# Kernel optimization log

Measured on AMD Instinct MI355X. Metric: run time of the kernel, lower is better.

The kernel has to match this reference:

```python
import jax, jax.numpy as jnp
import numpy as np

N = 50000      # nodes
E = 800000     # edges (before self-loops)
F_IN = 256     # feature_size
H = 96         # hidden_channels
G = 64         # graphs in batch
NC = 4         # num_classes
EPS = 1e-5     # BatchNorm eps


def _lrelu(x, s=0.01):
    return jnp.where(x >= 0, x, s * x)


def _gat(x, W, a_s, a_d, b, src, dst):
    # PyG GATConv, heads=1: linear transform, edge-wise LeakyReLU(0.2) scores,
    # segment softmax over destination nodes, scatter-add aggregation.
    h = x @ W                                                  # [N,H]
    e = _lrelu((h * a_s).sum(-1)[src] + (h * a_d).sum(-1)[dst], 0.2)  # [E+N]
    m = jax.ops.segment_max(e, dst, num_segments=N)
    ee = jnp.exp(e - m[dst])
    denom = jax.ops.segment_sum(ee, dst, num_segments=N)
    alpha = ee / denom[dst]
    return jax.ops.segment_sum(alpha[:, None] * h[src], dst, num_segments=N) + b


def _bn(x, g, b):
    # training-mode BatchNorm over the node dimension
    mu = x.mean(0)
    var = ((x - mu) ** 2).mean(0)
    return g * (x - mu) / jnp.sqrt(var + EPS) + b


def setup_inputs() -> dict:
    key = jax.random.key(0)
    ks = jax.random.split(key, 20)
    p = lambda i, sh: jax.random.normal(ks[i], sh, jnp.float32) * 0.05
    inp = {
        "x": jax.random.normal(ks[0], (N, F_IN), jnp.float32),
        "edge_index": jax.random.randint(ks[1], (2, E), 0, N),
        "batch": jnp.sort(jax.random.randint(ks[2], (N,), 0, G)),
        "embed_W": p(3, (F_IN, H)), "embed_b": jnp.zeros((H,), jnp.float32),
        "conv1_W": p(4, (H, H)), "conv1_as": p(5, (H,)), "conv1_ad": p(6, (H,)), "conv1_b": jnp.zeros((H,), jnp.float32),
        "conv2_W": p(7, (H, H)), "conv2_as": p(8, (H,)), "conv2_ad": p(9, (H,)), "conv2_b": jnp.zeros((H,), jnp.float32),
        "conv3_W": p(10, (H, H)), "conv3_as": p(11, (H,)), "conv3_ad": p(12, (H,)), "conv3_b": jnp.zeros((H,), jnp.float32),
        "fc1_W": p(13, (H, H)), "fc1_b": jnp.zeros((H,), jnp.float32),
        "fc2_W": p(14, (H, H)), "fc2_b": jnp.zeros((H,), jnp.float32),
        "bn1_g": jnp.ones((H,), jnp.float32), "bn1_b": jnp.zeros((H,), jnp.float32),
        "bn2_g": jnp.ones((H,), jnp.float32), "bn2_b": jnp.zeros((H,), jnp.float32),
        "bn3_g": jnp.ones((H,), jnp.float32), "bn3_b": jnp.zeros((H,), jnp.float32),
        "fc3_W": p(15, (H, H // 2)), "fc3_b": jnp.zeros((H // 2,), jnp.float32),
        "fc4_W": p(16, (H // 2, NC)), "fc4_b": jnp.zeros((NC,), jnp.float32),
    }
    return inp


def reference(x, edge_index, batch, embed_W, embed_b,
              conv1_W, conv1_as, conv1_ad, conv1_b,
              conv2_W, conv2_as, conv2_ad, conv2_b,
              conv3_W, conv3_as, conv3_ad, conv3_b,
              fc1_W, fc1_b, fc2_W, fc2_b,
              bn1_g, bn1_b, bn2_g, bn2_b, bn3_g, bn3_b,
              fc3_W, fc3_b, fc4_W, fc4_b):
    loops = jnp.arange(N)
    src = jnp.concatenate([edge_index[0], loops])   # GATConv add_self_loops=True
    dst = jnp.concatenate([edge_index[1], loops])

    h = _lrelu(x @ embed_W + embed_b)
    identity = h
    h = _lrelu(_bn(_gat(h, conv1_W, conv1_as, conv1_ad, conv1_b, src, dst), bn1_g, bn1_b)) + identity
    h = _lrelu(h @ fc1_W + fc1_b)
    h = _lrelu(_bn(_gat(h, conv2_W, conv2_as, conv2_ad, conv2_b, src, dst), bn2_g, bn2_b)) + identity
    h = _lrelu(h @ fc2_W + fc2_b)
    h = _lrelu(_bn(_gat(h, conv3_W, conv3_as, conv3_ad, conv3_b, src, dst), bn3_g, bn3_b)) + identity

    # Poincare ball expmap0 with c=1: tanh(||u||) * u / ||u||
    n = jnp.maximum(jnp.linalg.norm(h, axis=-1, keepdims=True), 1e-15)
    h = jnp.tanh(n) * h / n

    cnt = jax.ops.segment_sum(jnp.ones((N,), h.dtype), batch, num_segments=G)
    pooled = jax.ops.segment_sum(h, batch, num_segments=G) / jnp.maximum(cnt, 1.0)[:, None]

    o = _lrelu(pooled @ fc3_W + fc3_b)
    return o @ fc4_W + fc4_b
```

## Files before the change

### kernel.cpp

```cpp
#include <hip/hip_runtime.h>
#include <hip/hip_bf16.h>

#define DEVINL __device__ __forceinline__

constexpr int N_NODES = 50000;
constexpr int N_EDGES = 800000;
constexpr int F_IN    = 256;
constexpr int H       = 96;
constexpr int NG      = 64;
constexpr float BN_EPS = 1e-5f;
constexpr int SLOT    = 64;
constexpr int NREP    = 8;
constexpr int REPSZ   = NG * H + NG;
constexpr int BNREP   = 64;

constexpr int NBLK1 = 160;
constexpr int EPT1  = N_EDGES / NBLK1;
constexpr int NBUCK = 391;
constexpr int BCAP  = 64;
constexpr int NPACK = 276;

typedef short bf16x8 __attribute__((ext_vector_type(8)));
typedef float f32x4  __attribute__((ext_vector_type(4)));
typedef unsigned int u32x4 __attribute__((ext_vector_type(4)));

DEVINL float bf2f(unsigned int u) {
    union { unsigned int i; float f; } c; c.i = u << 16; return c.f;
}
DEVINL unsigned short f2bf(float f) {
    union { float f; unsigned int i; } c; c.f = f;
    unsigned int x = c.i;
    return (unsigned short)((x + 0x7fffu + ((x >> 16) & 1u)) >> 16);
}
DEVINL float lrelu01(float v) { return v >= 0.f ? v : 0.01f * v; }
DEVINL float ldf(const void* p, size_t i, int f32) {
    return f32 ? ((const float*)p)[i] : bf2f(((const unsigned short*)p)[i]);
}
DEVINL u32x4 ntld4(const void* p) {
    return __builtin_nontemporal_load((const u32x4*)p);
}

__global__ __launch_bounds__(256) void setup_k(
    const unsigned short* __restrict__ x,
    int* __restrict__ flag,
    const int* __restrict__ ei, uint2* __restrict__ bbuf,
    int* __restrict__ bcnt,
    const void* __restrict__ sE, const void* __restrict__ s0,
    const void* __restrict__ s1, const void* __restrict__ s2,
    const void* __restrict__ s3, const void* __restrict__ s4,
    unsigned short* __restrict__ dE, unsigned short* __restrict__ d0,
    unsigned short* __restrict__ d1, unsigned short* __restrict__ d2,
    unsigned short* __restrict__ d3, unsigned short* __restrict__ d4)
{
    __shared__ int lcur[NBUCK];

    if ((int)blockIdx.x >= NPACK) {
        int blk = (int)blockIdx.x - NPACK;
        for (int i = threadIdx.x; i < NBUCK; i += 256) lcur[i] = 0;
        __syncthreads();
        int base = blk * EPT1;
        int end  = base + EPT1;
        for (int e = base + (int)threadIdx.x; e < end; e += 256) {
            int sv = __builtin_nontemporal_load(ei + e);
            int dv = __builtin_nontemporal_load(ei + N_EDGES + e);
            int b  = dv >> 7;
            int pos = atomicAdd(&lcur[b], 1);
            if (pos < BCAP)
                bbuf[((size_t)blk * NBUCK + b) * BCAP + pos] =
                    make_uint2((unsigned)sv, (unsigned)dv);
        }
        __syncthreads();
        for (int i = threadIdx.x; i < NBUCK; i += 256)
            bcnt[blk * NBUCK + i] = min(lcur[i], BCAP);
        return;
    }

    if (blockIdx.x == 0 && threadIdx.x < 64) {
        int l = threadIdx.x;
        float f = bf2f(x[l]);
        bool huge = !(fabsf(f) <= 1e4f);
        unsigned long long m = __ballot(huge);
        if (l == 0) flag[0] = (__popcll(m) >= 8) ? 1 : 0;
    }
    float ff = bf2f(x[threadIdx.x & 63]);
    bool huge = !(fabsf(ff) <= 1e4f);
    unsigned long long mm = __ballot(huge);
    int lf32 = (__popcll(mm) >= 8) ? 1 : 0;

    int bb = blockIdx.x;
    const void* src; unsigned short* dst; int K, i0;
    if (bb < 96) { src = sE; dst = dE; K = F_IN; i0 = bb * 256; }
    else {
        int m = (bb - 96) / 36, r = (bb - 96) % 36;
        K = H; i0 = r * 256;
        if      (m == 0) { src = s0; dst = d0; }
        else if (m == 1) { src = s1; dst = d1; }
        else if (m == 2) { src = s2; dst = d2; }
        else if (m == 3) { src = s3; dst = d3; }
        else             { src = s4; dst = d4; }
    }
    int i = i0 + threadIdx.x;
    if (i >= K * 96) return;
    int c   = i / 3072;
    int rem = i - c * 3072;
    int t    = rem >> 9;
    int rem2 = rem & 511;
    int l = rem2 >> 3, j = rem2 & 7;
    int k = c * 32 + (l >> 4) * 8 + j;
    int n = t * 16 + (l & 15);
    if (lf32) dst[i] = f2bf(((const float*)src)[k * 96 + n]);
    else      dst[i] = ((const unsigned short*)src)[k * 96 + n];
}

__global__ __launch_bounds__(256, 4) void embconv_k(
    const void* __restrict__ xp, const unsigned short* __restrict__ WpkE,
    const void* __restrict__ embB, const unsigned short* __restrict__ Wcv,
    const int* __restrict__ dflag,
    unsigned short* __restrict__ ident, unsigned short* __restrict__ out,
    const void* __restrict__ as_, const void* __restrict__ ad_,
    float* __restrict__ s, float* __restrict__ d,
    const uint2* __restrict__ bbuf, const int* __restrict__ bcnt,
    unsigned short* __restrict__ col, int* __restrict__ fill,
    float* __restrict__ bnsumR, int M)
{
    union SMem {
        struct {
            unsigned short slots[128][SLOT];
            int lcnt[128];
            int ccnt[NBLK1];
        } c;
        unsigned short R[64][104];
    };
    __shared__ SMem sm;

    {
        int zi = blockIdx.x * 256 + threadIdx.x;
        if (zi < BNREP * 192) bnsumR[zi] = 0.f;
    }

    if ((int)blockIdx.x < NBUCK) {
        int b = blockIdx.x, tid = threadIdx.x;
        if (tid < 128) sm.c.lcnt[tid] = 0;
        for (int i = tid; i < NBLK1; i += 256) sm.c.ccnt[i] = bcnt[i * NBUCK + b];
        __syncthreads();

        int n0 = b << 7;
        for (int g = tid; g < NBLK1 * BCAP; g += 256) {
            int blk = g >> 6;
            int i   = g & (BCAP - 1);
            if (i < sm.c.ccnt[blk]) {
                uint2 e = bbuf[((size_t)blk * NBUCK + b) * BCAP + i];
                int local = (int)e.y - n0;
                int slot = atomicAdd(&sm.c.lcnt[local], 1);
                if (slot < SLOT) sm.c.slots[local][slot] = (unsigned short)e.x;
            }
        }
        __syncthreads();

        const uint4* ls = (const uint4*)sm.c.slots;
        for (int i = tid; i < 128 * 8; i += 256) {
            int node = n0 + (i >> 3);
            if (node < N_NODES)
                ((uint4*)col)[(size_t)node * 8 + (i & 7)] = ls[i];
        }
        if (tid < 128) {
            int node = n0 + tid;
            if (node < N_NODES) fill[node] = sm.c.lcnt[tid];
        }
        return;
    }

    const int gb   = (int)blockIdx.x - NBUCK;
    const int f32  = dflag[0];
    const int l    = threadIdx.x & 63;
    const int wave = threadIdx.x >> 6;
    const int row0 = gb * 64 + wave * 16;
    const int m    = l & 15;
    const int q    = l >> 4;
    const int arow = row0 + m;
    const bool aok = arow < M;

    bf16x8 av[8];
    #pragma unroll
    for (int c = 0; c < 8; c++) {
        bf16x8 a = {};
        if (aok) {
            if (f32) {
                const float* A = (const float*)xp + (size_t)arow * F_IN + c * 32 + q * 8;
                u32x4 u0 = ntld4(A);
                u32x4 u1 = ntld4(A + 4);
                #pragma unroll
                for (int j = 0; j < 4; j++) a[j]     = (short)f2bf(__uint_as_float(u0[j]));
                #pragma unroll
                for (int j = 0; j < 4; j++) a[4 + j] = (short)f2bf(__uint_as_float(u1[j]));
            } else {
                union { u32x4 u; bf16x8 h; } cv;
                cv.u = ntld4((const unsigned short*)xp + (size_t)arow * F_IN + c * 32 + q * 8);
                a = cv.h;
            }
        }
        av[c] = a;
    }

    f32x4 acc[6] = {};
    const bf16x8* wp1 = (const bf16x8*)WpkE;
    #pragma unroll
    for (int c = 0; c < 8; c++) {
        const int base = c * 384 + l;
        #pragma unroll
        for (int t = 0; t < 6; t++)
            acc[t] = __builtin_amdgcn_mfma_f32_16x16x32_bf16(av[c], wp1[base + t * 64], acc[t], 0, 0, 0);
    }

    float bv[6];
    #pragma unroll
    for (int t = 0; t < 6; t++) bv[t] = ldf(embB, t * 16 + m, f32);
    #pragma unroll
    for (int r = 0; r < 4; r++) {
        int lr = wave * 16 + q * 4 + r;
        int rr = row0 + q * 4 + r;
        #pragma unroll
        for (int t = 0; t < 6; t++) {
            unsigned short sv = f2bf(lrelu01(acc[t][r] + bv[t]));
            sm.R[lr][t * 16 + m] = sv;
            if (rr < M) ident[(size_t)rr * 96 + m + t * 16] = sv;
        }
    }
    __syncthreads();

    bf16x8 a2[3];
    #pragma unroll
    for (int c = 0; c < 3; c++)
        a2[c] = *(const bf16x8*)&sm.R[wave * 16 + m][c * 32 + q * 8];

    f32x4 acc2[6] = {};
    const bf16x8* wp2 = (const bf16x8*)Wcv;
    #pragma unroll
    for (int c = 0; c < 3; c++) {
        const int base = c * 384 + l;
        #pragma unroll
        for (int t = 0; t < 6; t++)
            acc2[t] = __builtin_amdgcn_mfma_f32_16x16x32_bf16(a2[c], wp2[base + t * 64], acc2[t], 0, 0, 0);
    }

    #pragma unroll
    for (int r = 0; r < 4; r++) {
        int rr = row0 + q * 4 + r;
        if (rr >= M) continue;
        size_t o = (size_t)rr * 96 + m;
        #pragma unroll
        for (int t = 0; t < 6; t++)
            out[o + t * 16] = f2bf(acc2[t][r]);
    }

    float asv[6], adv[6];
    #pragma unroll
    for (int t = 0; t < 6; t++) {
        asv[t] = ldf(as_, t * 16 + m, f32);
        adv[t] = ldf(ad_, t * 16 + m, f32);
    }
    #pragma unroll
    for (int r = 0; r < 4; r++) {
        float ps = 0.f, pd = 0.f;
        #pragma unroll
        for (int t = 0; t < 6; t++) {
            ps = fmaf(acc2[t][r], asv[t], ps);
            pd = fmaf(acc2[t][r], adv[t], pd);
        }
        #pragma unroll
        for (int off = 1; off < 16; off <<= 1) {
            ps += __shfl_xor(ps, off);
            pd += __shfl_xor(pd, off);
        }
        int rr = row0 + q * 4 + r;
        if (m == 0 && rr < M) { s[rr] = ps; d[rr] = pd; }
    }
}

__global__ __launch_bounds__(256, 4) void fcconv_k(
    const unsigned short* __restrict__ Ap,
    const unsigned short* __restrict__ Wfc, const void* __restrict__ bfc,
    const unsigned short* __restrict__ Wcv,
    const int* __restrict__ dflag,
    unsigned short* __restrict__ out,
    const void* __restrict__ as_, const void* __restrict__ ad_,
    float* __restrict__ s, float* __restrict__ d,
    const float* __restrict__ coefp, const unsigned short* __restrict__ idn,
    float* __restrict__ bnsumR, int M)
{
    __shared__ unsigned short R[64][104];

    {
        int zi = blockIdx.x * 256 + threadIdx.x;
        if (zi < BNREP * 192) bnsumR[zi] = 0.f;
    }

    const int wf32 = dflag[0];
    const int l    = threadIdx.x & 63;
    const int wave = threadIdx.x >> 6;
    const int row0 = blockIdx.x * 64 + wave * 16;
    const int m    = l & 15;
    const int q    = l >> 4;
    const int arow = row0 + m;
    const bool aok = arow < M;

    bf16x8 av[3];
    #pragma unroll
    for (int c = 0; c < 3; c++) {
        bf16x8 a = {};
        if (aok) {
            const int f0 = c * 32 + q * 8;
            uint4 xu = *(const uint4*)(Ap  + (size_t)arow * H + f0);
            uint4 iu = *(const uint4*)(idn + (size_t)arow * H + f0);
            unsigned int xs[4] = { xu.x, xu.y, xu.z, xu.w };
            unsigned int is[4] = { iu.x, iu.y, iu.z, iu.w };
            #pragma unroll
            for (int jj = 0; jj < 4; jj++) {
                int f = f0 + 2 * jj;
                float v0 = lrelu01(bf2f(xs[jj] & 0xffff) * coefp[f]     + coefp[96 + f])     + bf2f(is[jj] & 0xffff);
                float v1 = lrelu01(bf2f(xs[jj] >> 16)    * coefp[f + 1] + coefp[96 + f + 1]) + bf2f(is[jj] >> 16);
                a[2 * jj]     = (short)f2bf(v0);
                a[2 * jj + 1] = (short)f2bf(v1);
            }
        }
        av[c] = a;
    }

    f32x4 acc[6] = {};
    const bf16x8* wp1 = (const bf16x8*)Wfc;
    #pragma unroll
    for (int c = 0; c < 3; c++) {
        const int base = c * 384 + l;
        #pragma unroll
        for (int t = 0; t < 6; t++)
            acc[t] = __builtin_amdgcn_mfma_f32_16x16x32_bf16(av[c], wp1[base + t * 64], acc[t], 0, 0, 0);
    }

    float bv[6];
    #pragma unroll
    for (int t = 0; t < 6; t++) bv[t] = ldf(bfc, t * 16 + m, wf32);
    #pragma unroll
    for (int r = 0; r < 4; r++) {
        int lr = wave * 16 + q * 4 + r;
        #pragma unroll
        for (int t = 0; t < 6; t++)
            R[lr][t * 16 + m] = f2bf(lrelu01(acc[t][r] + bv[t]));
    }
    __syncthreads();

    bf16x8 a2[3];
    #pragma unroll
    for (int c = 0; c < 3; c++)
        a2[c] = *(const bf16x8*)&R[wave * 16 + m][c * 32 + q * 8];

    f32x4 acc2[6] = {};
    const bf16x8* wp2 = (const bf16x8*)Wcv;
    #pragma unroll
    for (int c = 0; c < 3; c++) {
        const int base = c * 384 + l;
        #pragma unroll
        for (int t = 0; t < 6; t++)
            acc2[t] = __builtin_amdgcn_mfma_f32_16x16x32_bf16(a2[c], wp2[base + t * 64], acc2[t], 0, 0, 0);
    }

    #pragma unroll
    for (int r = 0; r < 4; r++) {
        int rr = row0 + q * 4 + r;
        if (rr >= M) continue;
        size_t o = (size_t)rr * 96 + m;
        #pragma unroll
        for (int t = 0; t < 6; t++)
            out[o + t * 16] = f2bf(acc2[t][r]);
    }

    float asv[6], adv[6];
    #pragma unroll
    for (int t = 0; t < 6; t++) {
        asv[t] = ldf(as_, t * 16 + m, wf32);
        adv[t] = ldf(ad_, t * 16 + m, wf32);
    }
    #pragma unroll
    for (int r = 0; r < 4; r++) {
        float ps = 0.f, pd = 0.f;
        #pragma unroll
        for (int t = 0; t < 6; t++) {
            ps = fmaf(acc2[t][r], asv[t], ps);
            pd = fmaf(acc2[t][r], adv[t], pd);
        }
        #pragma unroll
        for (int off = 1; off < 16; off <<= 1) {
            ps += __shfl_xor(ps, off);
            pd += __shfl_xor(pd, off);
        }
        int rr = row0 + q * 4 + r;
        if (m == 0 && rr < M) { s[rr] = ps; d[rr] = pd; }
    }
}

__global__ __launch_bounds__(256) void agg_k(
    const unsigned short* __restrict__ h2, const float* __restrict__ s,
    const float* __restrict__ d, const int* __restrict__ fill,
    const unsigned short* __restrict__ col, const void* __restrict__ bias,
    const int* __restrict__ dflag, unsigned short* __restrict__ out,
    float* __restrict__ bnsumR, float* __restrict__ zp, int M)
{
    __shared__ uint2 uwb[4][80];
    __shared__ float lstat[4][192];
    if (zp) {
        int zi = blockIdx.x * 256 + threadIdx.x;
        if (zi < NREP * REPSZ) zp[zi] = 0.f;
    }
    int f32 = dflag[0];
    int v = (blockIdx.x * blockDim.x + threadIdx.x) >> 6;
    int l = threadIdx.x & 63;
    int wv = threadIdx.x >> 6;
    bool act = v < M;
    bool hw = (l < 48);
    int  c2 = 2 * l;
    float o0 = 0.f, o1 = 0.f;

    if (act) {
        int st   = v * SLOT;
        int degr = min(fill[v], SLOT - 1);
        int deg  = degr + 1;

        float dv = d[v];
        int u = 0; float e = -1e30f;
        if (l < degr) {
            u = col[st + l];
            float t = s[u] + dv;
            e = t >= 0.f ? t : 0.2f * t;
        } else if (l == degr) {
            u = v;
            float t = s[v] + dv;
            e = t >= 0.f ? t : 0.2f * t;
        }
        float lm = e;
        #pragma unroll
        for (int off = 32; off > 0; off >>= 1) lm = fmaxf(lm, __shfl_xor(lm, off));
        float w = (l < deg) ? __expf(e - lm) : 0.f;
        float lsum = w;
        #pragma unroll
        for (int off = 32; off > 0; off >>= 1) lsum += __shfl_xor(lsum, off);
        float rden = 1.0f / lsum;

        uwb[wv][l] = make_uint2((unsigned int)u, __float_as_uint(w));
        if (l < 16) uwb[wv][64 + l] = make_uint2(0u, 0u);

        float a0 = 0.f, a1 = 0.f;
        const uint2* myuw = uwb[wv];
        for (int j = 0; j < deg; j += 16) {
            int lim = deg - j;
            uint2 p[16];
            #pragma unroll
            for (int k = 0; k < 16; k++) p[k] = myuw[j + k];
            if (hw) {
                unsigned int hv[16];
                #pragma unroll
                for (int k = 0; k < 16; k++)
                    hv[k] = (k < lim) ? *(const unsigned int*)(h2 + (size_t)p[k].x * 96 + c2) : 0u;
                #pragma unroll
                for (int k = 0; k < 16; k++) {
                    float wj = __uint_as_float(p[k].y);
                    a0 = fmaf(wj, bf2f(hv[k] & 0xffff), a0);
                    a1 = fmaf(wj, bf2f(hv[k] >> 16),    a1);
                }
            }
        }
        if (hw) {
            float b0 = ldf(bias, c2,     f32);
            float b1 = ldf(bias, c2 + 1, f32);
            unsigned int o = (unsigned int)f2bf(a0 * rden + b0)
                           | ((unsigned int)f2bf(a1 * rden + b1) << 16);
            *(unsigned int*)(out + (size_t)v * 96 + c2) = o;
            o0 = bf2f(o & 0xffff);
            o1 = bf2f(o >> 16);
        }
    }

    if (hw) {
        lstat[wv][c2]          = o0;
        lstat[wv][c2 + 1]      = o1;
        lstat[wv][96 + c2]     = o0 * o0;
        lstat[wv][97 + c2]     = o1 * o1;
    }
    __syncthreads();
    if (threadIdx.x < 192) {
        float tot = lstat[0][threadIdx.x] + lstat[1][threadIdx.x]
                  + lstat[2][threadIdx.x] + lstat[3][threadIdx.x];
        atomicAdd(&bnsumR[(blockIdx.x & (BNREP - 1)) * 192 + threadIdx.x], tot);
    }
}

__global__ void bncoef_k(const float* __restrict__ bnsumR,
                         const void* __restrict__ g_,
                         const void* __restrict__ b_,
                         const int* __restrict__ dflag,
                         float* __restrict__ coef)
{
    __shared__ float tot[192];
    int t = threadIdx.x;
    if (t < 192) {
        float s = 0.f;
        #pragma unroll 8
        for (int r = 0; r < BNREP; r++) s += bnsumR[r * 192 + t];
        tot[t] = s;
    }
    __syncthreads();
    if (t < 96) {
        int f32 = dflag[0];
        float mu  = tot[t] * (1.f / N_NODES);
        float var = tot[96 + t] * (1.f / N_NODES) - mu * mu;
        float rinv = 1.0f / sqrtf(var + BN_EPS);
        float sc = ldf(g_, t, f32) * rinv;
        coef[t]      = sc;
        coef[96 + t] = ldf(b_, t, f32) - mu * sc;
    }
}

__global__ __launch_bounds__(256) void bnpool_k(
    const unsigned short* __restrict__ h, const float* __restrict__ coef,
    const unsigned short* __restrict__ iden, const int* __restrict__ batch,
    float* __restrict__ pooled8, int M)
{
    int w = (blockIdx.x * blockDim.x + threadIdx.x) >> 6;
    int l = threadIdx.x & 63;
    int v0 = w * 16;
    if (v0 >= M) return;
    float* P = pooled8 + (blockIdx.x & (NREP - 1)) * REPSZ;
    float* C = P + NG * H;
    bool hw = (l < 48);
    int  c2 = 2 * l;
    float sc0 = 0.f, sc1 = 0.f, sh0 = 0.f, sh1 = 0.f;
    if (hw) {
        sc0 = coef[c2]; sc1 = coef[c2 + 1];
        sh0 = coef[96 + c2]; sh1 = coef[97 + c2];
    }
    int nv = min(16, M - v0);

    int gb[16];
    #pragma unroll
    for (int k = 0; k < 16; k++) gb[k] = batch[v0 + min(k, nv - 1)];

    float x0[16], x1[16], q[16];
    #pragma unroll
    for (int k = 0; k < 16; k++) { x0[k] = 0.f; x1[k] = 0.f; q[k] = 0.f; }
    if (hw) {
        unsigned int xu[16], iu[16];
        #pragma unroll
        for (int k = 0; k < 16; k++) {
            int v = v0 + k;
            if (k < nv) {
                xu[k] = *(const unsigned int*)(h    + (size_t)v * 96 + c2);
                iu[k] = *(const unsigned int*)(iden + (size_t)v * 96 + c2);
            } else { xu[k] = 0u; iu[k] = 0u; }
        }
        #pragma unroll
        for (int k = 0; k < 16; k++) {
            x0[k] = lrelu01(bf2f(xu[k] & 0xffff) * sc0 + sh0) + bf2f(iu[k] & 0xffff);
            x1[k] = lrelu01(bf2f(xu[k] >> 16)    * sc1 + sh1) + bf2f(iu[k] >> 16);
            q[k]  = x0[k] * x0[k] + x1[k] * x1[k];
        }
    }

    #pragma unroll
    for (int off = 32; off > 0; off >>= 1) {
        #pragma unroll
        for (int k = 0; k < 16; k++) q[k] += __shfl_xor(q[k], off);
    }

    float f[16];
    #pragma unroll
    for (int k = 0; k < 16; k++) {
        float n = fmaxf(sqrtf(q[k]), 1e-15f);
        if (n < 15.f) {
            float t = __expf(2.f * n);
            f[k] = (t - 1.f) / ((t + 1.f) * n);
        } else {
            f[k] = 1.f / n;
        }
    }

    float a0 = 0.f, a1 = 0.f, cnt = 0.f;
    int curg = -1;
    for (int k = 0; k < nv; k++) {
        int g = gb[k];
        if (g != curg) {
            if (curg >= 0) {
                if (hw) {
                    atomicAdd(&P[curg * 96 + c2],     a0);
                    atomicAdd(&P[curg * 96 + c2 + 1], a1);
                }
                if (l == 0) atomicAdd(&C[curg], cnt);
            }
            a0 = a1 = 0.f; cnt = 0.f; curg = g;
        }
        a0 = fmaf(f[k], x0[k], a0);
        a1 = fmaf(f[k], x1[k], a1);
        cnt += 1.f;
    }
    if (curg >= 0) {
        if (hw) {
            atomicAdd(&P[curg * 96 + c2],     a0);
            atomicAdd(&P[curg * 96 + c2 + 1], a1);
        }
        if (l == 0) atomicAdd(&C[curg], cnt);
    }
}

__global__ __launch_bounds__(64) void head_k(const float* __restrict__ pooled8,
                                             const void* __restrict__ w3,
                                             const void* __restrict__ b3,
                                             const void* __restrict__ w4,
                                             const void* __restrict__ b4,
                                             const int* __restrict__ dflag,
                                             void* __restrict__ outv)
{
    int g = blockIdx.x;
    int t = threadIdx.x;
    int f32 = dflag[0];
    __shared__ float p[96];
    __shared__ float o[48];
    float cs = 0.f;
    #pragma unroll
    for (int r = 0; r < NREP; r++) cs += pooled8[r * REPSZ + NG * H + g];
    float inv = 1.0f / fmaxf(cs, 1.0f);
    for (int c = t; c < 96; c += 64) {
        float v = 0.f;
        #pragma unroll
        for (int r = 0; r < NREP; r++) v += pooled8[r * REPSZ + g * 96 + c];
        p[c] = v * inv;
    }
    __syncthreads();
    if (t < 48) {
        float a = ldf(b3, t, f32);
        #pragma unroll
        for (int c = 0; c < 96; c++) a = fmaf(p[c], ldf(w3, (size_t)c * 48 + t, f32), a);
        o[t] = lrelu01(a);
    }
    __syncthreads();
    if (t < 4) {
        float a = ldf(b4, t, f32);
        #pragma unroll
        for (int j = 0; j < 48; j++) a = fmaf(o[j], ldf(w4, j * 4 + t, f32), a);
        if (f32) ((float*)outv)[g * 4 + t] = a;
        else     ((unsigned short*)outv)[g * 4 + t] = f2bf(a);
    }
}

extern "C" void kernel_launch(void* const* d_in, const int* in_sizes, int n_in,
                              void* d_out, int out_size, void* d_ws, size_t ws_size,
                              hipStream_t stream)
{
    const void* x     = d_in[0];
    const int*  ei    = (const int*)d_in[1];
    const int*  batch = (const int*)d_in[2];
    const void* embW  = d_in[3];
    const void* embB  = d_in[4];
    const void* convW[3]  = { d_in[5],  d_in[9],  d_in[13] };
    const void* convAs[3] = { d_in[6],  d_in[10], d_in[14] };
    const void* convAd[3] = { d_in[7],  d_in[11], d_in[15] };
    const void* convB[3]  = { d_in[8],  d_in[12], d_in[16] };
    const void* fcW[2]    = { d_in[17], d_in[19] };
    const void* fcB[2]    = { d_in[18], d_in[20] };
    const void* bnG[3]    = { d_in[21], d_in[23], d_in[25] };
    const void* bnB[3]    = { d_in[22], d_in[24], d_in[26] };
    const void* fc3W = d_in[27];
    const void* fc3b = d_in[28];
    const void* fc4W = d_in[29];
    const void* fc4b = d_in[30];

    char* wp_ = (char*)d_ws;
    auto alloc = [&](size_t b) { char* p = wp_; wp_ += (b + 255) & ~(size_t)255; return p; };
    int*   dflag = (int*)alloc(256);
    unsigned short* ident = (unsigned short*)alloc((size_t)N_NODES * H * 2);
    unsigned short* hA    = (unsigned short*)alloc((size_t)N_NODES * H * 2);
    unsigned short* hB    = (unsigned short*)alloc((size_t)N_NODES * H * 2);
    float* s_sc  = (float*)alloc((size_t)N_NODES * 4);
    float* d_sc  = (float*)alloc((size_t)N_NODES * 4);
    float* bnsumR = (float*)alloc((size_t)BNREP * 192 * 4);
    float* coef  = (float*)alloc(192 * 4);
    float* pooled8 = (float*)alloc((size_t)NREP * REPSZ * 4);
    int*   fill  = (int*)alloc((size_t)N_NODES * 4);
    unsigned short* col = (unsigned short*)alloc((size_t)N_NODES * SLOT * 2);
    uint2* bbuf = (uint2*)alloc((size_t)NBLK1 * NBUCK * BCAP * 8);
    int*   bcnt = (int*)alloc((size_t)NBLK1 * NBUCK * 4);
    unsigned short* wpkEmb = (unsigned short*)alloc((size_t)F_IN * 96 * 2);
    unsigned short* wpkS[5];
    for (int i = 0; i < 5; i++) wpkS[i] = (unsigned short*)alloc((size_t)H * 96 * 2);

    const int GM = (N_NODES + 63) / 64;
    const int GW = (N_NODES * 64 + 255) / 256;
    const int GP = ((N_NODES + 15) / 16 * 64 + 255) / 256;

    setup_k<<<NPACK + NBLK1, 256, 0, stream>>>(
        (const unsigned short*)x, dflag,
        ei, bbuf, bcnt,
        embW, convW[0], convW[1], convW[2], fcW[0], fcW[1],
        wpkEmb, wpkS[0], wpkS[1], wpkS[2], wpkS[3], wpkS[4]);

    embconv_k<<<NBUCK + GM, 256, 0, stream>>>(
        x, wpkEmb, embB, wpkS[0], dflag, ident, hB,
        convAs[0], convAd[0], s_sc, d_sc,
        bbuf, bcnt, col, fill, bnsumR, N_NODES);

    agg_k<<<GW, 256, 0, stream>>>(hB, s_sc, d_sc, fill, col, convB[0], dflag, hA,
                                  bnsumR, nullptr, N_NODES);
    bncoef_k<<<1, 192, 0, stream>>>(bnsumR, bnG[0], bnB[0], dflag, coef);
    fcconv_k<<<GM, 256, 0, stream>>>(hA, wpkS[3], fcB[0], wpkS[1], dflag, hB,
                                     convAs[1], convAd[1], s_sc, d_sc,
                                     coef, ident, bnsumR, N_NODES);

    agg_k<<<GW, 256, 0, stream>>>(hB, s_sc, d_sc, fill, col, convB[1], dflag, hA,
                                  bnsumR, nullptr, N_NODES);
    bncoef_k<<<1, 192, 0, stream>>>(bnsumR, bnG[1], bnB[1], dflag, coef);
    fcconv_k<<<GM, 256, 0, stream>>>(hA, wpkS[4], fcB[1], wpkS[2], dflag, hB,
                                     convAs[2], convAd[2], s_sc, d_sc,
                                     coef, ident, bnsumR, N_NODES);

    agg_k<<<GW, 256, 0, stream>>>(hB, s_sc, d_sc, fill, col, convB[2], dflag, hA,
                                  bnsumR, pooled8, N_NODES);
    bncoef_k<<<1, 192, 0, stream>>>(bnsumR, bnG[2], bnB[2], dflag, coef);

    bnpool_k<<<GP, 256, 0, stream>>>(hA, coef, ident, batch, pooled8, N_NODES);
    head_k<<<NG, 64, 0, stream>>>(pooled8, fc3W, fc3b, fc4W, fc4b, dflag, d_out);
}
```

Measured before the change: 356.7 us.

## Fold BN coefficient kernel into consumers and broadcast edge weights via shuffles

Removes the three single-block bncoef_k launches: each fcconv_k and bnpool_k block now reduces the replicated BN partial sums and computes scale/shift into shared memory. The BN sum buffers are double-buffered so a consumer can read the previous layer's sums while zeroing the next layer's buffer. In agg_k, neighbor indices and softmax weights are broadcast with wave shuffles instead of being staged through shared memory, and the self-loop handling is merged into one branch. The trade-off is redundant per-block reduction of 64x192 floats plus extra barriers in every consumer block, in exchange for fewer launches and serial gaps.

```diff
diff --git a/kernel.cpp b/kernel.cpp
--- a/kernel.cpp
+++ b/kernel.cpp
@@ -38,6 +38,31 @@
 }
 DEVINL u32x4 ntld4(const void* p) {
     return __builtin_nontemporal_load((const u32x4*)p);
+}
+
+DEVINL void coef_from_sums(float* lcoef, const float* __restrict__ bnsumRd,
+                           const void* __restrict__ g_, const void* __restrict__ b_,
+                           int f32)
+{
+    int t = threadIdx.x;
+    if (t < 192) {
+        float ssum = 0.f;
+        #pragma unroll 8
+        for (int r = 0; r < BNREP; r++) ssum += bnsumRd[r * 192 + t];
+        lcoef[t] = ssum;
+    }
+    __syncthreads();
+    float sc = 0.f, sh = 0.f;
+    if (t < 96) {
+        float mu  = lcoef[t] * (1.f / N_NODES);
+        float var = lcoef[96 + t] * (1.f / N_NODES) - mu * mu;
+        float rinv = 1.0f / sqrtf(var + BN_EPS);
+        sc = ldf(g_, t, f32) * rinv;
+        sh = ldf(b_, t, f32) - mu * sc;
+    }
+    __syncthreads();
+    if (t < 96) { lcoef[t] = sc; lcoef[96 + t] = sh; }
+    __syncthreads();
 }
 
 __global__ __launch_bounds__(256) void setup_k(
@@ -121,7 +146,7 @@
     float* __restrict__ s, float* __restrict__ d,
     const uint2* __restrict__ bbuf, const int* __restrict__ bcnt,
     unsigned short* __restrict__ col, int* __restrict__ fill,
-    float* __restrict__ bnsumR, int M)
+    float* __restrict__ bnsumZ, int M)
 {
     union SMem {
         struct {
@@ -135,7 +160,7 @@
 
     {
         int zi = blockIdx.x * 256 + threadIdx.x;
-        if (zi < BNREP * 192) bnsumR[zi] = 0.f;
+        if (zi < BNREP * 192) bnsumZ[zi] = 0.f;
     }
 
     if ((int)blockIdx.x < NBUCK) {
@@ -285,17 +310,22 @@
     unsigned short* __restrict__ out,
     const void* __restrict__ as_, const void* __restrict__ ad_,
     float* __restrict__ s, float* __restrict__ d,
-    const float* __restrict__ coefp, const unsigned short* __restrict__ idn,
-    float* __restrict__ bnsumR, int M)
+    const void* __restrict__ g_, const void* __restrict__ b_,
+    const float* __restrict__ bnsumRd,
+    const unsigned short* __restrict__ idn,
+    float* __restrict__ bnsumZ, int M)
 {
     __shared__ unsigned short R[64][104];
+    __shared__ float lcoef[192];
 
     {
         int zi = blockIdx.x * 256 + threadIdx.x;
-        if (zi < BNREP * 192) bnsumR[zi] = 0.f;
+        if (zi < BNREP * 192) bnsumZ[zi] = 0.f;
     }
 
     const int wf32 = dflag[0];
+    coef_from_sums(lcoef, bnsumRd, g_, b_, wf32);
+
     const int l    = threadIdx.x & 63;
     const int wave = threadIdx.x >> 6;
     const int row0 = blockIdx.x * 64 + wave * 16;
@@ -317,8 +347,8 @@
             #pragma unroll
             for (int jj = 0; jj < 4; jj++) {
                 int f = f0 + 2 * jj;
-                float v0 = lrelu01(bf2f(xs[jj] & 0xffff) * coefp[f]     + coefp[96 + f])     + bf2f(is[jj] & 0xffff);
-                float v1 = lrelu01(bf2f(xs[jj] >> 16)    * coefp[f + 1] + coefp[96 + f + 1]) + bf2f(is[jj] >> 16);
+                float v0 = lrelu01(bf2f(xs[jj] & 0xffff) * lcoef[f]     + lcoef[96 + f])     + bf2f(is[jj] & 0xffff);
+                float v1 = lrelu01(bf2f(xs[jj] >> 16)    * lcoef[f + 1] + lcoef[97 + f]) + bf2f(is[jj] >> 16);
                 a[2 * jj]     = (short)f2bf(v0);
                 a[2 * jj + 1] = (short)f2bf(v1);
             }
@@ -404,7 +434,6 @@
     const int* __restrict__ dflag, unsigned short* __restrict__ out,
     float* __restrict__ bnsumR, float* __restrict__ zp, int M)
 {
-    __shared__ uint2 uwb[4][80];
     __shared__ float lstat[4][192];
     if (zp) {
         int zi = blockIdx.x * 256 + threadIdx.x;
@@ -425,14 +454,11 @@
         int deg  = degr + 1;
 
         float dv = d[v];
-        int u = 0; float e = -1e30f;
-        if (l < degr) {
-            u = col[st + l];
+        int u = v;
+        if (l < degr) u = col[st + l];
+        float e = -1e30f;
+        if (l < deg) {
             float t = s[u] + dv;
-            e = t >= 0.f ? t : 0.2f * t;
-        } else if (l == degr) {
-            u = v;
-            float t = s[v] + dv;
             e = t >= 0.f ? t : 0.2f * t;
         }
         float lm = e;
@@ -444,27 +470,21 @@
         for (int off = 32; off > 0; off >>= 1) lsum += __shfl_xor(lsum, off);
         float rden = 1.0f / lsum;
 
-        uwb[wv][l] = make_uint2((unsigned int)u, __float_as_uint(w));
-        if (l < 16) uwb[wv][64 + l] = make_uint2(0u, 0u);
-
         float a0 = 0.f, a1 = 0.f;
-        const uint2* myuw = uwb[wv];
         for (int j = 0; j < deg; j += 16) {
             int lim = deg - j;
-            uint2 p[16];
+            unsigned int hv[16];
             #pragma unroll
-            for (int k = 0; k < 16; k++) p[k] = myuw[j + k];
-            if (hw) {
-                unsigned int hv[16];
-                #pragma unroll
-                for (int k = 0; k < 16; k++)
-                    hv[k] = (k < lim) ? *(const unsigned int*)(h2 + (size_t)p[k].x * 96 + c2) : 0u;
-                #pragma unroll
-                for (int k = 0; k < 16; k++) {
-                    float wj = __uint_as_float(p[k].y);
-                    a0 = fmaf(wj, bf2f(hv[k] & 0xffff), a0);
-                    a1 = fmaf(wj, bf2f(hv[k] >> 16),    a1);
-                }
+            for (int k = 0; k < 16; k++) {
+                int uk = __shfl(u, j + k);
+                hv[k] = (hw && k < lim)
+                      ? *(const unsigned int*)(h2 + (size_t)uk * 96 + c2) : 0u;
+            }
+            #pragma unroll
+            for (int k = 0; k < 16; k++) {
+                float wk = __shfl(w, j + k);
+                a0 = fmaf(wk, bf2f(hv[k] & 0xffff), a0);
+                a1 = fmaf(wk, bf2f(hv[k] >> 16),    a1);
             }
         }
         if (hw) {
@@ -492,37 +512,16 @@
     }
 }
 
-__global__ void bncoef_k(const float* __restrict__ bnsumR,
-                         const void* __restrict__ g_,
-                         const void* __restrict__ b_,
-                         const int* __restrict__ dflag,
-                         float* __restrict__ coef)
-{
-    __shared__ float tot[192];
-    int t = threadIdx.x;
-    if (t < 192) {
-        float s = 0.f;
-        #pragma unroll 8
-        for (int r = 0; r < BNREP; r++) s += bnsumR[r * 192 + t];
-        tot[t] = s;
-    }
-    __syncthreads();
-    if (t < 96) {
-        int f32 = dflag[0];
-        float mu  = tot[t] * (1.f / N_NODES);
-        float var = tot[96 + t] * (1.f / N_NODES) - mu * mu;
-        float rinv = 1.0f / sqrtf(var + BN_EPS);
-        float sc = ldf(g_, t, f32) * rinv;
-        coef[t]      = sc;
-        coef[96 + t] = ldf(b_, t, f32) - mu * sc;
-    }
-}
-
 __global__ __launch_bounds__(256) void bnpool_k(
-    const unsigned short* __restrict__ h, const float* __restrict__ coef,
+    const unsigned short* __restrict__ h,
+    const void* __restrict__ g_, const void* __restrict__ b_,
+    const float* __restrict__ bnsumRd, const int* __restrict__ dflag,
     const unsigned short* __restrict__ iden, const int* __restrict__ batch,
     float* __restrict__ pooled8, int M)
 {
+    __shared__ float lcoef[192];
+    coef_from_sums(lcoef, bnsumRd, g_, b_, dflag[0]);
+
     int w = (blockIdx.x * blockDim.x + threadIdx.x) >> 6;
     int l = threadIdx.x & 63;
     int v0 = w * 16;
@@ -533,8 +532,8 @@
     int  c2 = 2 * l;
     float sc0 = 0.f, sc1 = 0.f, sh0 = 0.f, sh1 = 0.f;
     if (hw) {
-        sc0 = coef[c2]; sc1 = coef[c2 + 1];
-        sh0 = coef[96 + c2]; sh1 = coef[97 + c2];
+        sc0 = lcoef[c2]; sc1 = lcoef[c2 + 1];
+        sh0 = lcoef[96 + c2]; sh1 = lcoef[97 + c2];
     }
     int nv = min(16, M - v0);
 
@@ -678,8 +677,8 @@
     unsigned short* hB    = (unsigned short*)alloc((size_t)N_NODES * H * 2);
     float* s_sc  = (float*)alloc((size_t)N_NODES * 4);
     float* d_sc  = (float*)alloc((size_t)N_NODES * 4);
-    float* bnsumR = (float*)alloc((size_t)BNREP * 192 * 4);
-    float* coef  = (float*)alloc(192 * 4);
+    float* bnsumA = (float*)alloc((size_t)BNREP * 192 * 4);
+    float* bnsumB = (float*)alloc((size_t)BNREP * 192 * 4);
     float* pooled8 = (float*)alloc((size_t)NREP * REPSZ * 4);
     int*   fill  = (int*)alloc((size_t)N_NODES * 4);
     unsigned short* col = (unsigned short*)alloc((size_t)N_NODES * SLOT * 2);
@@ -702,26 +701,24 @@
     embconv_k<<<NBUCK + GM, 256, 0, stream>>>(
         x, wpkEmb, embB, wpkS[0], dflag, ident, hB,
         convAs[0], convAd[0], s_sc, d_sc,
-        bbuf, bcnt, col, fill, bnsumR, N_NODES);
+        bbuf, bcnt, col, fill, bnsumA, N_NODES);
 
     agg_k<<<GW, 256, 0, stream>>>(hB, s_sc, d_sc, fill, col, convB[0], dflag, hA,
-                                  bnsumR, nullptr, N_NODES);
-    bncoef_k<<<1, 192, 0, stream>>>(bnsumR, bnG[0], bnB[0], dflag, coef);
+                                  bnsumA, nullptr, N_NODES);
     fcconv_k<<<GM, 256, 0, stream>>>(hA, wpkS[3], fcB[0], wpkS[1], dflag, hB,
                                      convAs[1], convAd[1], s_sc, d_sc,
-                                     coef, ident, bnsumR, N_NODES);
+                                     bnG[0], bnB[0], bnsumA, ident, bnsumB, N_NODES);
 
     agg_k<<<GW, 256, 0, stream>>>(hB, s_sc, d_sc, fill, col, convB[1], dflag, hA,
-                                  bnsumR, nullptr, N_NODES);
-    bncoef_k<<<1, 192, 0, stream>>>(bnsumR, bnG[1], bnB[1], dflag, coef);
+                                  bnsumB, nullptr, N_NODES);
     fcconv_k<<<GM, 256, 0, stream>>>(hA, wpkS[4], fcB[1], wpkS[2], dflag, hB,
                                      convAs[2], convAd[2], s_sc, d_sc,
-                                     coef, ident, bnsumR, N_NODES);
+                                     bnG[1], bnB[1], bnsumB, ident, bnsumA, N_NODES);
 
     agg_k<<<GW, 256, 0, stream>>>(hB, s_sc, d_sc, fill, col, convB[2], dflag, hA,
-                                  bnsumR, pooled8, N_NODES);
-    bncoef_k<<<1, 192, 0, stream>>>(bnsumR, bnG[2], bnB[2], dflag, coef);
-
-    bnpool_k<<<GP, 256, 0, stream>>>(hA, coef, ident, batch, pooled8, N_NODES);
+                                  bnsumA, pooled8, N_NODES);
+
+    bnpool_k<<<GP, 256, 0, stream>>>(hA, bnG[2], bnB[2], bnsumA, dflag,
+                                     ident, batch, pooled8, N_NODES);
     head_k<<<NG, 64, 0, stream>>>(pooled8, fc3W, fc3b, fc4W, fc4b, dflag, d_out);
 }
```

After: 369.0 us. 3.5% more time.
